# Kernel optimization log

Measured on AMD Instinct MI355X. Metric: run time of the kernel, lower is better.

## Reference

```python
import jax, jax.numpy as jnp
import numpy as np

NUM_ITEMS = 100000
HIDDEN = 128
NNZ = 1600000


def setup_inputs() -> dict:
    key = jax.random.key(0)
    k1, k2, k3, k4, k5, k6 = jax.random.split(key, 6)
    item_embedding_table = jax.random.normal(k1, (NUM_ITEMS, HIDDEN), dtype=jnp.float32)
    adj_rows = jnp.sort(jax.random.randint(k2, (NNZ,), 0, NUM_ITEMS, dtype=jnp.int32))
    adj_cols = jax.random.randint(k3, (NNZ,), 0, NUM_ITEMS, dtype=jnp.int32)
    adj_vals = jax.random.uniform(k4, (NNZ,), dtype=jnp.float32)
    # nn.Linear default init (uniform in +-1/sqrt(fan_in)) approximated by scaled normal
    W_weight = jax.random.normal(k5, (HIDDEN, HIDDEN), dtype=jnp.float32) / np.sqrt(HIDDEN)
    W_bias = jax.random.normal(k6, (HIDDEN,), dtype=jnp.float32) * 0.01
    return {
        "item_embedding_table": item_embedding_table,
        "adj_rows": adj_rows,
        "adj_cols": adj_cols,
        "adj_vals": adj_vals,
        "W_weight": W_weight,
        "W_bias": W_bias,
    }


def reference(item_embedding_table, adj_rows, adj_cols, adj_vals, W_weight, W_bias):
    # support = W(x): x @ W^T + b   (nn.Linear convention: weight [out, in])
    support = jnp.einsum("nd,hd->nh", item_embedding_table, W_weight) + W_bias  # [N, H]
    # output = sparse_coo(adj) @ support, via gather + segment-sum scatter
    msgs = adj_vals[:, None] * support[adj_cols]  # [nnz, H]
    output = jax.ops.segment_sum(msgs, adj_rows, num_segments=NUM_ITEMS)  # [N, H]
    return output
```

## Files before the change

kernel.cpp:

```cpp
#include <hip/hip_runtime.h>

#define N_ITEMS 100000
#define HID 128
#define NNZ_T 1600000

typedef unsigned short ushort_t;
typedef unsigned int uint_t;
typedef short bf16x8 __attribute__((ext_vector_type(8)));
typedef float f32x4 __attribute__((ext_vector_type(4)));

static __device__ __forceinline__ ushort_t f32_to_bf16(float f) {
    uint_t u = __float_as_uint(f);
    uint_t r = (u + 0x7FFFu + ((u >> 16) & 1u)) >> 16;
    return (ushort_t)r;
}

__global__ void prep_w(const float* __restrict__ W, ushort_t* __restrict__ Wb) {
    int i = blockIdx.x * blockDim.x + threadIdx.x;
    Wb[i] = f32_to_bf16(W[i]);
}

__global__ void build_rowptr(const int* __restrict__ rows, int* __restrict__ row_ptr) {
    int r = blockIdx.x * blockDim.x + threadIdx.x;
    if (r > N_ITEMS) return;
    int lo = 0, hi = NNZ_T;
    while (lo < hi) {
        int mid = (lo + hi) >> 1;
        if (rows[mid] < r) lo = mid + 1; else hi = mid;
    }
    row_ptr[r] = lo;
}

__global__ __launch_bounds__(256) void gemm_mfma(
    const float* __restrict__ X, const ushort_t* __restrict__ Wb,
    const float* __restrict__ bias, ushort_t* __restrict__ S) {
    const int lane = threadIdx.x & 63;
    const int wave = threadIdx.x >> 6;
    const int m = lane & 15;
    const int q = lane >> 4;
    const int row0 = blockIdx.x * 64 + wave * 16;

    int arow = row0 + m;
    if (arow >= N_ITEMS) arow = N_ITEMS - 1;

    f32x4 acc[8] = {};

#pragma unroll
    for (int kb = 0; kb < 4; ++kb) {
        const int k0 = kb * 32 + q * 8;
        float4 a0 = *(const float4*)&X[(size_t)arow * HID + k0];
        float4 a1 = *(const float4*)&X[(size_t)arow * HID + k0 + 4];
        bf16x8 af;
        af[0] = (short)f32_to_bf16(a0.x); af[1] = (short)f32_to_bf16(a0.y);
        af[2] = (short)f32_to_bf16(a0.z); af[3] = (short)f32_to_bf16(a0.w);
        af[4] = (short)f32_to_bf16(a1.x); af[5] = (short)f32_to_bf16(a1.y);
        af[6] = (short)f32_to_bf16(a1.z); af[7] = (short)f32_to_bf16(a1.w);
#pragma unroll
        for (int nt = 0; nt < 8; ++nt) {
            bf16x8 bfr = *(const bf16x8*)&Wb[(size_t)(nt * 16 + m) * HID + k0];
            acc[nt] = __builtin_amdgcn_mfma_f32_16x16x32_bf16(af, bfr, acc[nt], 0, 0, 0);
        }
    }

#pragma unroll
    for (int nt = 0; nt < 8; ++nt) {
        const int col = nt * 16 + m;
        const float bv = bias[col];
#pragma unroll
        for (int r = 0; r < 4; ++r) {
            const int row = row0 + q * 4 + r;
            if (row < N_ITEMS)
                S[(size_t)row * HID + col] = f32_to_bf16(acc[nt][r] + bv);
        }
    }
}

__global__ __launch_bounds__(256) void spmm_csr(
    const int* __restrict__ cols, const float* __restrict__ vals,
    const int* __restrict__ row_ptr, const ushort_t* __restrict__ S,
    float* __restrict__ out) {
    const int lane = threadIdx.x & 63;
    const int row = blockIdx.x * 4 + (int)__builtin_amdgcn_readfirstlane(threadIdx.x >> 6);
    if (row >= N_ITEMS) return;

    const int p0 = row_ptr[row];
    const int p1 = row_ptr[row + 1];

    float2 acc = make_float2(0.f, 0.f);
    int p = p0;
    for (; p + 8 <= p1; p += 8) {
        uint_t u[8]; float v[8];
#pragma unroll
        for (int j = 0; j < 8; ++j) {
            int c = cols[p + j];
            v[j] = vals[p + j];
            u[j] = *(const uint_t*)&S[(size_t)c * HID + 2 * lane];
        }
#pragma unroll
        for (int j = 0; j < 8; ++j) {
            acc.x = fmaf(v[j], __uint_as_float(u[j] << 16), acc.x);
            acc.y = fmaf(v[j], __uint_as_float(u[j] & 0xFFFF0000u), acc.y);
        }
    }
    for (; p < p1; ++p) {
        int c = cols[p];
        float v = vals[p];
        uint_t u = *(const uint_t*)&S[(size_t)c * HID + 2 * lane];
        acc.x = fmaf(v, __uint_as_float(u << 16), acc.x);
        acc.y = fmaf(v, __uint_as_float(u & 0xFFFF0000u), acc.y);
    }
    *(float2*)&out[(size_t)row * HID + 2 * lane] = acc;
}

extern "C" void kernel_launch(void* const* d_in, const int* in_sizes, int n_in,
                              void* d_out, int out_size, void* d_ws, size_t ws_size,
                              hipStream_t stream) {
    const float* X    = (const float*)d_in[0];
    const int*   rows = (const int*)  d_in[1];
    const int*   cols = (const int*)  d_in[2];
    const float* vals = (const float*)d_in[3];
    const float* W    = (const float*)d_in[4];
    const float* bias = (const float*)d_in[5];
    float* out = (float*)d_out;

    ushort_t* Wb      = (ushort_t*)d_ws;
    ushort_t* S       = Wb + HID * HID;
    int*      row_ptr = (int*)(S + (size_t)N_ITEMS * HID);

    prep_w<<<(HID * HID) / 256, 256, 0, stream>>>(W, Wb);
    build_rowptr<<<(N_ITEMS + 256) / 256, 256, 0, stream>>>(rows, row_ptr);
    gemm_mfma<<<(N_ITEMS + 63) / 64, 256, 0, stream>>>(X, Wb, bias, S);
    spmm_csr<<<(N_ITEMS + 3) / 4, 256, 0, stream>>>(cols, vals, row_ptr, S, out);
}
```

Before: 222.6 us.

## Merge prep kernels, vectorize GEMM epilogue, split SpMM rows across lane groups

Result: faster. 215.6 us (-3.1%).

```diff
diff --git a/kernel.cpp b/kernel.cpp
--- a/kernel.cpp
+++ b/kernel.cpp
@@ -3,6 +3,8 @@
 #define N_ITEMS 100000
 #define HID 128
 #define NNZ_T 1600000
+#define PREPW_BLOCKS 64
+#define RP_BLOCKS 391
 
 typedef unsigned short ushort_t;
 typedef unsigned int uint_t;
@@ -15,13 +17,14 @@
     return (ushort_t)r;
 }
 
-__global__ void prep_w(const float* __restrict__ W, ushort_t* __restrict__ Wb) {
-    int i = blockIdx.x * blockDim.x + threadIdx.x;
-    Wb[i] = f32_to_bf16(W[i]);
-}
-
-__global__ void build_rowptr(const int* __restrict__ rows, int* __restrict__ row_ptr) {
-    int r = blockIdx.x * blockDim.x + threadIdx.x;
+__global__ void prep(const float* __restrict__ W, const int* __restrict__ rows,
+                     ushort_t* __restrict__ Wb, int* __restrict__ row_ptr) {
+    if (blockIdx.x < PREPW_BLOCKS) {
+        int i = blockIdx.x * 256 + threadIdx.x;
+        Wb[i] = f32_to_bf16(W[i]);
+        return;
+    }
+    int r = (blockIdx.x - PREPW_BLOCKS) * 256 + threadIdx.x;
     if (r > N_ITEMS) return;
     int lo = 0, hi = NNZ_T;
     while (lo < hi) {
@@ -50,28 +53,32 @@
         const int k0 = kb * 32 + q * 8;
         float4 a0 = *(const float4*)&X[(size_t)arow * HID + k0];
         float4 a1 = *(const float4*)&X[(size_t)arow * HID + k0 + 4];
-        bf16x8 af;
-        af[0] = (short)f32_to_bf16(a0.x); af[1] = (short)f32_to_bf16(a0.y);
-        af[2] = (short)f32_to_bf16(a0.z); af[3] = (short)f32_to_bf16(a0.w);
-        af[4] = (short)f32_to_bf16(a1.x); af[5] = (short)f32_to_bf16(a1.y);
-        af[6] = (short)f32_to_bf16(a1.z); af[7] = (short)f32_to_bf16(a1.w);
+        bf16x8 xf;
+        xf[0] = (short)f32_to_bf16(a0.x); xf[1] = (short)f32_to_bf16(a0.y);
+        xf[2] = (short)f32_to_bf16(a0.z); xf[3] = (short)f32_to_bf16(a0.w);
+        xf[4] = (short)f32_to_bf16(a1.x); xf[5] = (short)f32_to_bf16(a1.y);
+        xf[6] = (short)f32_to_bf16(a1.z); xf[7] = (short)f32_to_bf16(a1.w);
 #pragma unroll
         for (int nt = 0; nt < 8; ++nt) {
-            bf16x8 bfr = *(const bf16x8*)&Wb[(size_t)(nt * 16 + m) * HID + k0];
-            acc[nt] = __builtin_amdgcn_mfma_f32_16x16x32_bf16(af, bfr, acc[nt], 0, 0, 0);
+            bf16x8 wf = *(const bf16x8*)&Wb[(size_t)(nt * 16 + m) * HID + k0];
+            acc[nt] = __builtin_amdgcn_mfma_f32_16x16x32_bf16(wf, xf, acc[nt], 0, 0, 0);
         }
     }
 
+    const int srow = row0 + m;
+    const bool ok = srow < N_ITEMS;
 #pragma unroll
     for (int nt = 0; nt < 8; ++nt) {
-        const int col = nt * 16 + m;
-        const float bv = bias[col];
-#pragma unroll
-        for (int r = 0; r < 4; ++r) {
-            const int row = row0 + q * 4 + r;
-            if (row < N_ITEMS)
-                S[(size_t)row * HID + col] = f32_to_bf16(acc[nt][r] + bv);
-        }
+        const int c0 = nt * 16 + q * 4;
+        float4 bv = *(const float4*)&bias[c0];
+        ushort_t h0 = f32_to_bf16(acc[nt][0] + bv.x);
+        ushort_t h1 = f32_to_bf16(acc[nt][1] + bv.y);
+        ushort_t h2 = f32_to_bf16(acc[nt][2] + bv.z);
+        ushort_t h3 = f32_to_bf16(acc[nt][3] + bv.w);
+        uint2 pk;
+        pk.x = (uint_t)h0 | ((uint_t)h1 << 16);
+        pk.y = (uint_t)h2 | ((uint_t)h3 << 16);
+        if (ok) *(uint2*)&S[(size_t)srow * HID + c0] = pk;
     }
 }
 
@@ -80,36 +87,56 @@
     const int* __restrict__ row_ptr, const ushort_t* __restrict__ S,
     float* __restrict__ out) {
     const int lane = threadIdx.x & 63;
-    const int row = blockIdx.x * 4 + (int)__builtin_amdgcn_readfirstlane(threadIdx.x >> 6);
+    const int row = blockIdx.x * 4 + ((threadIdx.x >> 6) & 3);
     if (row >= N_ITEMS) return;
+
+    const int g = lane >> 4;
+    const int l = lane & 15;
 
     const int p0 = row_ptr[row];
     const int p1 = row_ptr[row + 1];
 
-    float2 acc = make_float2(0.f, 0.f);
-    int p = p0;
-    for (; p + 8 <= p1; p += 8) {
-        uint_t u[8]; float v[8];
+    float acc[8] = {};
+
+    if (p1 > p0) {
+        const int last = p1 - 1;
+        for (int p = p0; p < p1; p += 16) {
+            uint4 u[4]; float v[4];
 #pragma unroll
-        for (int j = 0; j < 8; ++j) {
-            int c = cols[p + j];
-            v[j] = vals[p + j];
-            u[j] = *(const uint_t*)&S[(size_t)c * HID + 2 * lane];
-        }
+            for (int t = 0; t < 4; ++t) {
+                int idx = p + 4 * t + g;
+                bool ok = idx < p1;
+                idx = min(idx, last);
+                int c = cols[idx];
+                v[t] = ok ? vals[idx] : 0.f;
+                u[t] = *(const uint4*)&S[(size_t)c * HID + 8 * l];
+            }
 #pragma unroll
-        for (int j = 0; j < 8; ++j) {
-            acc.x = fmaf(v[j], __uint_as_float(u[j] << 16), acc.x);
-            acc.y = fmaf(v[j], __uint_as_float(u[j] & 0xFFFF0000u), acc.y);
+            for (int t = 0; t < 4; ++t) {
+                acc[0] = fmaf(v[t], __uint_as_float(u[t].x << 16),          acc[0]);
+                acc[1] = fmaf(v[t], __uint_as_float(u[t].x & 0xFFFF0000u),  acc[1]);
+                acc[2] = fmaf(v[t], __uint_as_float(u[t].y << 16),          acc[2]);
+                acc[3] = fmaf(v[t], __uint_as_float(u[t].y & 0xFFFF0000u),  acc[3]);
+                acc[4] = fmaf(v[t], __uint_as_float(u[t].z << 16),          acc[4]);
+                acc[5] = fmaf(v[t], __uint_as_float(u[t].z & 0xFFFF0000u),  acc[5]);
+                acc[6] = fmaf(v[t], __uint_as_float(u[t].w << 16),          acc[6]);
+                acc[7] = fmaf(v[t], __uint_as_float(u[t].w & 0xFFFF0000u),  acc[7]);
+            }
         }
     }
-    for (; p < p1; ++p) {
-        int c = cols[p];
-        float v = vals[p];
-        uint_t u = *(const uint_t*)&S[(size_t)c * HID + 2 * lane];
-        acc.x = fmaf(v, __uint_as_float(u << 16), acc.x);
-        acc.y = fmaf(v, __uint_as_float(u & 0xFFFF0000u), acc.y);
+
+#pragma unroll
+    for (int e = 0; e < 8; ++e) {
+        acc[e] += __shfl_xor(acc[e], 16, 64);
+        acc[e] += __shfl_xor(acc[e], 32, 64);
     }
-    *(float2*)&out[(size_t)row * HID + 2 * lane] = acc;
+    if (g == 0) {
+        float4 o0 = make_float4(acc[0], acc[1], acc[2], acc[3]);
+        float4 o1 = make_float4(acc[4], acc[5], acc[6], acc[7]);
+        float* p = &out[(size_t)row * HID + 8 * l];
+        *(float4*)p = o0;
+        *(float4*)(p + 4) = o1;
+    }
 }
 
 extern "C" void kernel_launch(void* const* d_in, const int* in_sizes, int n_in,
@@ -127,8 +154,7 @@
     ushort_t* S       = Wb + HID * HID;
     int*      row_ptr = (int*)(S + (size_t)N_ITEMS * HID);
 
-    prep_w<<<(HID * HID) / 256, 256, 0, stream>>>(W, Wb);
-    build_rowptr<<<(N_ITEMS + 256) / 256, 256, 0, stream>>>(rows, row_ptr);
+    prep<<<PREPW_BLOCKS + RP_BLOCKS, 256, 0, stream>>>(W, rows, Wb, row_ptr);
     gemm_mfma<<<(N_ITEMS + 63) / 64, 256, 0, stream>>>(X, Wb, bias, S);
     spmm_csr<<<(N_ITEMS + 3) / 4, 256, 0, stream>>>(cols, vals, row_ptr, S, out);
 }
```
